# Kernel tuning notes

Hardware: AMD Instinct MI355X
Metric: run time of the kernel (lower is better)

Reference implementation:

```python
import jax, jax.numpy as jnp
import numpy as np

B, N = 64, 512
D_ENT, H = 2000, 768
LN_EPS = 1e-12


def setup_inputs() -> dict:
    key = jax.random.key(0)
    ks = jax.random.split(key, 16)
    s = 1.0 / np.sqrt(D_ENT)
    sh = 1.0 / np.sqrt(H)
    return {
        "node_embeddings": jax.random.normal(ks[0], (B, N, D_ENT), jnp.float32),
        "node_types": jax.random.randint(ks[1], (B, N), 0, 2),
        "layers": jax.random.randint(ks[2], (B, N), 0, 8),
        "operators": jax.random.randint(ks[3], (B, N), 0, 2),
        "in_degs": jax.random.randint(ks[4], (B, N), 0, 8),
        "out_degs": jax.random.randint(ks[5], (B, N), 0, 8),
        "negs": jax.random.randint(ks[6], (B, N), 0, 2),
        "type_emb": jax.random.normal(ks[7], (2, H), jnp.float32),
        "layer_emb": jax.random.normal(ks[8], (8, H), jnp.float32),
        "op_emb": jax.random.normal(ks[9], (2, H), jnp.float32),
        "in_emb": jax.random.normal(ks[10], (8, H), jnp.float32),
        "out_emb": jax.random.normal(ks[11], (8, H), jnp.float32),
        "proj_w": jax.random.uniform(ks[12], (H, D_ENT), jnp.float32, -s, s),
        "proj_b": jnp.zeros((H,), jnp.float32),
        "neg_w": jax.random.uniform(ks[13], (H, H), jnp.float32, -sh, sh),
        "neg_b": jnp.zeros((H,), jnp.float32),
        "ln_g": jnp.ones((H,), jnp.float32),
        "ln_b": jnp.zeros((H,), jnp.float32),
    }


def reference(node_embeddings, node_types, layers, operators, in_degs, out_degs, negs,
              type_emb, layer_emb, op_emb, in_emb, out_emb,
              proj_w, proj_b, neg_w, neg_b, ln_g, ln_b):
    # linear projection: [B,N,D_ENT] @ [D_ENT,H]
    x = jnp.einsum("bnd,hd->bnh", node_embeddings, proj_w) + proj_b
    # summed small-table lookups
    x = x + type_emb[node_types] + layer_emb[layers] + op_emb[operators] \
        + in_emb[in_degs] + out_emb[out_degs]
    # rows with negs==1 go through MLP (single Linear h->h); masked select/scatter
    y = jnp.einsum("bnh,gh->bng", x, neg_w) + neg_b
    x = jnp.where((negs == 1)[..., None], y, x)
    # LayerNorm
    mu = jnp.mean(x, axis=-1, keepdims=True)
    var = jnp.mean(jnp.square(x - mu), axis=-1, keepdims=True)
    x = (x - mu) * jax.lax.rsqrt(var + LN_EPS) * ln_g + ln_b
    # dropout is identity in eval mode
    return x
```

## Files before the change

kernel.cpp:

```cpp
#include <hip/hip_runtime.h>
#include <stdint.h>

typedef unsigned short u16;
typedef short v8s __attribute__((ext_vector_type(8)));
typedef float v4f __attribute__((ext_vector_type(4)));

typedef __attribute__((address_space(1))) uint32_t g_u32;
typedef __attribute__((address_space(3))) uint32_t l_u32;

__device__ __forceinline__ void glds16(const void* g, void* l) {
    __builtin_amdgcn_global_load_lds((const g_u32*)g, (l_u32*)l, 16, 0, 0);
}

__device__ __forceinline__ u16 f2b(float f) {
    uint32_t u = __builtin_bit_cast(uint32_t, f);
    u += 0x7FFFu + ((u >> 16) & 1u);
    return (u16)(u >> 16);
}

__device__ __forceinline__ uint32_t pk2(float a, float b) {
    uint32_t ua = __builtin_bit_cast(uint32_t, a) + 0x8000u;
    uint32_t ub = __builtin_bit_cast(uint32_t, b) + 0x8000u;
    return __builtin_amdgcn_perm(ub, ua, 0x07060302u);
}

#define MTOT  32768
#define HDIM  768
#define KDIM  2000
#define KPAD  2016

__global__ __launch_bounds__(256) void cvt_weights(
    const float* __restrict__ pw, const float* __restrict__ nw,
    u16* __restrict__ Wb, u16* __restrict__ NWb)
{
    const int h = blockIdx.x;
    const float* src = pw + (size_t)h * KDIM;
    u16* dst = Wb + (size_t)h * KPAD;
    for (int k = threadIdx.x; k < KPAD; k += 256)
        dst[k] = (k < KDIM) ? f2b(src[k]) : (u16)0;
    const float* s2 = nw + (size_t)h * HDIM;
    u16* d2 = NWb + (size_t)h * HDIM;
    for (int k = threadIdx.x; k < HDIM; k += 256)
        d2[k] = f2b(s2[k]);
}

__global__ __launch_bounds__(512, 2) void gemm1(
    const float* __restrict__ A, const u16* __restrict__ Wb,
    const float* __restrict__ pb,
    const int* __restrict__ i_ty, const int* __restrict__ i_la,
    const int* __restrict__ i_op, const int* __restrict__ i_in, const int* __restrict__ i_ou,
    const float* __restrict__ te, const float* __restrict__ le, const float* __restrict__ oe,
    const float* __restrict__ ie, const float* __restrict__ ooe,
    u16* __restrict__ Xb)
{
    __shared__ __align__(16) float Asf[3][256 * 32];
    __shared__ __align__(16) u16  Bs[3][256 * 32];

    const int bid = blockIdx.x;
    const int s = bid >> 3;
    const int mt = (bid & 7) * 16 + s / 3;
    const int nt = s % 3;
    const int m_base = mt * 256, n_base = nt * 256;

    const int tid = threadIdx.x;
    const int w = tid >> 6, lane = tid & 63;
    const int lm = lane & 15, quad = lane >> 4;
    const int wm = (w >> 2) * 128, wn = (w & 3) * 64;

    const float* aRowBase[4];
    int aOff[4];
    int aBase[4];
#pragma unroll
    for (int t = 0; t < 4; t++) {
        const int rl = w * 32 + t * 8 + (lane >> 3);
        const int c16 = (lane & 7) ^ (rl & 7);
        aRowBase[t] = A + (size_t)(m_base + rl) * KDIM;
        aOff[t] = c16 * 4;
        aBase[t] = (w * 32 + t * 8) * 32;
    }
    const u16* bSrc[2];
    int bBase[2];
#pragma unroll
    for (int t = 0; t < 2; t++) {
        const int rl = w * 32 + t * 16 + (lane >> 2);
        const int c = (lane & 3) ^ ((rl >> 1) & 3);
        bSrc[t] = Wb + (size_t)(n_base + rl) * KPAD + c * 8;
        bBase[t] = (w * 32 + t * 16) * 32;
    }

    v4f acc[8][4];
#pragma unroll
    for (int i = 0; i < 8; i++)
#pragma unroll
        for (int j = 0; j < 4; j++) acc[i][j] = (v4f){0.f, 0.f, 0.f, 0.f};

    auto issue = [&](int kb) {
        const int sl = kb % 3;
#pragma unroll
        for (int t = 0; t < 4; t++) {
            int k = kb * 32 + aOff[t];
            k = (k > 1996) ? 1996 : k;
            glds16(aRowBase[t] + k, &Asf[sl][aBase[t]]);
        }
#pragma unroll
        for (int t = 0; t < 2; t++)
            glds16(bSrc[t] + kb * 32, &Bs[sl][bBase[t]]);
    };

    auto compute = [&](int kb) {
        const int sl = kb % 3;
        v8s af[8], bf[4];
#pragma unroll
        for (int i = 0; i < 8; i++) {
            const int r = wm + i * 16 + lm;
            const int sw = r & 7;
            const float4 lo = *(const float4*)&Asf[sl][r * 32 + (((2 * quad)     ^ sw) << 2)];
            const float4 hi = *(const float4*)&Asf[sl][r * 32 + (((2 * quad + 1) ^ sw) << 2)];
            int4 p;
            p.x = (int)pk2(lo.x, lo.y); p.y = (int)pk2(lo.z, lo.w);
            p.z = (int)pk2(hi.x, hi.y); p.w = (int)pk2(hi.z, hi.w);
            af[i] = __builtin_bit_cast(v8s, p);
        }
#pragma unroll
        for (int j = 0; j < 4; j++) {
            const int r = wn + j * 16 + lm;
            bf[j] = *(const v8s*)&Bs[sl][r * 32 + ((quad ^ ((r >> 1) & 3)) << 3)];
        }
#pragma unroll
        for (int i = 0; i < 8; i++)
#pragma unroll
            for (int j = 0; j < 4; j++)
                acc[i][j] = __builtin_amdgcn_mfma_f32_16x16x32_bf16(af[i], bf[j], acc[i][j], 0, 0, 0);
    };

    issue(0);
    issue(1);

    for (int kb = 0; kb < 61; ++kb) {
        asm volatile("s_waitcnt vmcnt(6)" ::: "memory");
        __builtin_amdgcn_s_barrier();
        __builtin_amdgcn_sched_barrier(0);
        issue(kb + 2);
        compute(kb);
    }
    asm volatile("s_waitcnt vmcnt(6)" ::: "memory");
    __builtin_amdgcn_s_barrier();
    __builtin_amdgcn_sched_barrier(0);
    compute(61);
    asm volatile("s_waitcnt vmcnt(0)" ::: "memory");
    __builtin_amdgcn_s_barrier();
    __builtin_amdgcn_sched_barrier(0);
    compute(62);

#pragma unroll
    for (int i = 0; i < 8; i++) {
#pragma unroll
        for (int r = 0; r < 4; r++) {
            const int row = m_base + wm + i * 16 + quad * 4 + r;
            const int ty = i_ty[row], la = i_la[row], op = i_op[row];
            const int di = i_in[row], doo = i_ou[row];
            const float* pte = te + (size_t)ty * HDIM;
            const float* ple = le + (size_t)la * HDIM;
            const float* poe = oe + (size_t)op * HDIM;
            const float* pie = ie + (size_t)di * HDIM;
            const float* pou = ooe + (size_t)doo * HDIM;
            u16* orow = Xb + (size_t)row * HDIM;
#pragma unroll
            for (int j = 0; j < 4; j++) {
                const int col = n_base + wn + j * 16 + lm;
                float v = acc[i][j][r] + pb[col] + pte[col] + ple[col] + poe[col] + pie[col] + pou[col];
                orow[col] = f2b(v);
            }
        }
    }
}

__global__ __launch_bounds__(512, 2) void gemm2(
    const u16* __restrict__ Xb, const u16* __restrict__ NWb,
    const float* __restrict__ nb, u16* __restrict__ Yb)
{
    __shared__ __align__(16) u16 As[3][256 * 32];
    __shared__ __align__(16) u16 Bs[3][256 * 32];

    const int bid = blockIdx.x;
    const int s = bid >> 3;
    const int mt = (bid & 7) * 16 + s / 3;
    const int nt = s % 3;
    const int m_base = mt * 256, n_base = nt * 256;

    const int tid = threadIdx.x;
    const int w = tid >> 6, lane = tid & 63;
    const int lm = lane & 15, quad = lane >> 4;
    const int wm = (w >> 2) * 128, wn = (w & 3) * 64;

    const u16* aSrc[2];
    const u16* bSrc[2];
    int sBase[2];
#pragma unroll
    for (int t = 0; t < 2; t++) {
        const int rl = w * 32 + t * 16 + (lane >> 2);
        const int c = (lane & 3) ^ ((rl >> 1) & 3);
        aSrc[t] = Xb  + (size_t)(m_base + rl) * HDIM + c * 8;
        bSrc[t] = NWb + (size_t)(n_base + rl) * HDIM + c * 8;
        sBase[t] = (w * 32 + t * 16) * 32;
    }

    v4f acc[8][4];
#pragma unroll
    for (int i = 0; i < 8; i++)
#pragma unroll
        for (int j = 0; j < 4; j++) acc[i][j] = (v4f){0.f, 0.f, 0.f, 0.f};

    auto issue = [&](int kb) {
        const int sl = kb % 3;
#pragma unroll
        for (int t = 0; t < 2; t++) {
            glds16(aSrc[t] + kb * 32, &As[sl][sBase[t]]);
            glds16(bSrc[t] + kb * 32, &Bs[sl][sBase[t]]);
        }
    };

    auto compute = [&](int kb) {
        const int sl = kb % 3;
        v8s af[8], bf[4];
#pragma unroll
        for (int i = 0; i < 8; i++) {
            const int r = wm + i * 16 + lm;
            af[i] = *(const v8s*)&As[sl][r * 32 + ((quad ^ ((r >> 1) & 3)) << 3)];
        }
#pragma unroll
        for (int j = 0; j < 4; j++) {
            const int r = wn + j * 16 + lm;
            bf[j] = *(const v8s*)&Bs[sl][r * 32 + ((quad ^ ((r >> 1) & 3)) << 3)];
        }
#pragma unroll
        for (int i = 0; i < 8; i++)
#pragma unroll
            for (int j = 0; j < 4; j++)
                acc[i][j] = __builtin_amdgcn_mfma_f32_16x16x32_bf16(af[i], bf[j], acc[i][j], 0, 0, 0);
    };

    issue(0);
    issue(1);

    for (int kb = 0; kb < 22; ++kb) {
        asm volatile("s_waitcnt vmcnt(4)" ::: "memory");
        __builtin_amdgcn_s_barrier();
        __builtin_amdgcn_sched_barrier(0);
        issue(kb + 2);
        compute(kb);
    }
    asm volatile("s_waitcnt vmcnt(4)" ::: "memory");
    __builtin_amdgcn_s_barrier();
    __builtin_amdgcn_sched_barrier(0);
    compute(22);
    asm volatile("s_waitcnt vmcnt(0)" ::: "memory");
    __builtin_amdgcn_s_barrier();
    __builtin_amdgcn_sched_barrier(0);
    compute(23);

#pragma unroll
    for (int i = 0; i < 8; i++) {
#pragma unroll
        for (int r = 0; r < 4; r++) {
            const int row = m_base + wm + i * 16 + quad * 4 + r;
            u16* orow = Yb + (size_t)row * HDIM;
#pragma unroll
            for (int j = 0; j < 4; j++) {
                const int col = n_base + wn + j * 16 + lm;
                orow[col] = f2b(acc[i][j][r] + nb[col]);
            }
        }
    }
}

__global__ __launch_bounds__(256) void ln_k(
    const u16* __restrict__ Xb, const u16* __restrict__ Yb,
    const int* __restrict__ negs,
    const float* __restrict__ g, const float* __restrict__ b,
    float* __restrict__ out)
{
    const int w = threadIdx.x >> 6, lane = threadIdx.x & 63;
    const int row = blockIdx.x * 4 + w;
    const u16* src = ((negs[row] == 1) ? Yb : Xb) + (size_t)row * HDIM;

    float v[12];
    float s = 0.f, ss = 0.f;
#pragma unroll
    for (int p = 0; p < 3; p++) {
        uint2 u = *(const uint2*)(src + (p * 64 + lane) * 4);
        float f0 = __builtin_bit_cast(float, u.x << 16);
        float f1 = __builtin_bit_cast(float, u.x & 0xFFFF0000u);
        float f2 = __builtin_bit_cast(float, u.y << 16);
        float f3 = __builtin_bit_cast(float, u.y & 0xFFFF0000u);
        v[p * 4 + 0] = f0; v[p * 4 + 1] = f1; v[p * 4 + 2] = f2; v[p * 4 + 3] = f3;
        s += f0 + f1 + f2 + f3;
        ss += f0 * f0 + f1 * f1 + f2 * f2 + f3 * f3;
    }
#pragma unroll
    for (int off = 1; off < 64; off <<= 1) {
        s += __shfl_xor(s, off);
        ss += __shfl_xor(ss, off);
    }
    const float mean = s * (1.f / (float)HDIM);
    const float var = ss * (1.f / (float)HDIM) - mean * mean;
    const float rs = rsqrtf(var + 1e-12f);

    float* orow = out + (size_t)row * HDIM;
#pragma unroll
    for (int p = 0; p < 3; p++) {
        const int c0 = (p * 64 + lane) * 4;
        float4 gg = *(const float4*)(g + c0);
        float4 bb = *(const float4*)(b + c0);
        float4 o;
        o.x = (v[p * 4 + 0] - mean) * rs * gg.x + bb.x;
        o.y = (v[p * 4 + 1] - mean) * rs * gg.y + bb.y;
        o.z = (v[p * 4 + 2] - mean) * rs * gg.z + bb.z;
        o.w = (v[p * 4 + 3] - mean) * rs * gg.w + bb.w;
        *(float4*)(orow + c0) = o;
    }
}

extern "C" void kernel_launch(void* const* d_in, const int* in_sizes, int n_in,
                              void* d_out, int out_size, void* d_ws, size_t ws_size,
                              hipStream_t stream) {
    (void)in_sizes; (void)n_in; (void)out_size; (void)ws_size;
    const float* A   = (const float*)d_in[0];
    const int* i_ty  = (const int*)d_in[1];
    const int* i_la  = (const int*)d_in[2];
    const int* i_op  = (const int*)d_in[3];
    const int* i_in  = (const int*)d_in[4];
    const int* i_ou  = (const int*)d_in[5];
    const int* negs  = (const int*)d_in[6];
    const float* te  = (const float*)d_in[7];
    const float* le  = (const float*)d_in[8];
    const float* oe  = (const float*)d_in[9];
    const float* ie  = (const float*)d_in[10];
    const float* ooe = (const float*)d_in[11];
    const float* pw  = (const float*)d_in[12];
    const float* pb  = (const float*)d_in[13];
    const float* nw  = (const float*)d_in[14];
    const float* nb  = (const float*)d_in[15];
    const float* lng = (const float*)d_in[16];
    const float* lnb = (const float*)d_in[17];
    float* out = (float*)d_out;

    char* ws = (char*)d_ws;
    u16* Wb  = (u16*)ws;
    u16* NWb = (u16*)(ws + 3096576);
    u16* Xb  = (u16*)(ws + 3096576 + 1179648);
    u16* Yb  = (u16*)(ws + 3096576 + 1179648 + 50331648);

    cvt_weights<<<768, 256, 0, stream>>>(pw, nw, Wb, NWb);
    gemm1<<<384, 512, 0, stream>>>(A, Wb, pb, i_ty, i_la, i_op, i_in, i_ou,
                                   te, le, oe, ie, ooe, Xb);
    gemm2<<<384, 512, 0, stream>>>(Xb, NWb, nb, Yb);
    ln_k<<<8192, 256, 0, stream>>>(Xb, Yb, negs, lng, lnb, out);
}
```

Baseline: 773.2 us.

## Restructure both GEMMs into 8-phase double-buffered K=64 pipelines with register-staged A conversion

Both GEMM kernels move from a triple-buffered K=32 loop to double-buffered K=64 tiles, and each K-step is split into quadrant phases that interleave loads with MFMA bursts raised with s_setprio. In gemm1 the fp32 A tile is now loaded into registers and converted to bf16 once before the LDS write, instead of staging fp32 in LDS and packing at every fragment read. This halves A's LDS footprint and conversion traffic. Weight padding grows to 2048 so K tiles align, and block-to-tile swizzling changes. The cost is more registers for staged A, more barriers per tile, and a hand-tuned vmcnt schedule that could be fragile.

```diff
diff --git a/kernel.cpp b/kernel.cpp
--- a/kernel.cpp
+++ b/kernel.cpp
@@ -11,13 +11,11 @@
 __device__ __forceinline__ void glds16(const void* g, void* l) {
     __builtin_amdgcn_global_load_lds((const g_u32*)g, (l_u32*)l, 16, 0, 0);
 }
-
 __device__ __forceinline__ u16 f2b(float f) {
     uint32_t u = __builtin_bit_cast(uint32_t, f);
     u += 0x7FFFu + ((u >> 16) & 1u);
     return (u16)(u >> 16);
 }
-
 __device__ __forceinline__ uint32_t pk2(float a, float b) {
     uint32_t ua = __builtin_bit_cast(uint32_t, a) + 0x8000u;
     uint32_t ub = __builtin_bit_cast(uint32_t, b) + 0x8000u;
@@ -27,7 +25,11 @@
 #define MTOT  32768
 #define HDIM  768
 #define KDIM  2000
-#define KPAD  2016
+#define KP2   2048
+
+#define BARX do { __builtin_amdgcn_s_barrier(); __builtin_amdgcn_sched_barrier(0); } while (0)
+#define VMW(n) asm volatile("s_waitcnt vmcnt(" #n ")" ::: "memory")
+#define LGKM0  asm volatile("s_waitcnt lgkmcnt(0)" ::: "memory")
 
 __global__ __launch_bounds__(256) void cvt_weights(
     const float* __restrict__ pw, const float* __restrict__ nw,
@@ -35,8 +37,8 @@
 {
     const int h = blockIdx.x;
     const float* src = pw + (size_t)h * KDIM;
-    u16* dst = Wb + (size_t)h * KPAD;
-    for (int k = threadIdx.x; k < KPAD; k += 256)
+    u16* dst = Wb + (size_t)h * KP2;
+    for (int k = threadIdx.x; k < KP2; k += 256)
         dst[k] = (k < KDIM) ? f2b(src[k]) : (u16)0;
     const float* s2 = nw + (size_t)h * HDIM;
     u16* d2 = NWb + (size_t)h * HDIM;
@@ -53,13 +55,12 @@
     const float* __restrict__ ie, const float* __restrict__ ooe,
     u16* __restrict__ Xb)
 {
-    __shared__ __align__(16) float Asf[3][256 * 32];
-    __shared__ __align__(16) u16  Bs[3][256 * 32];
+    __shared__ __align__(16) u16 As[2][256 * 64];
+    __shared__ __align__(16) u16 Bs[2][256 * 64];
 
     const int bid = blockIdx.x;
-    const int s = bid >> 3;
-    const int mt = (bid & 7) * 16 + s / 3;
-    const int nt = s % 3;
+    const int sw = (bid & 7) * 48 + (bid >> 3);
+    const int mt = sw / 3, nt = sw % 3;
     const int m_base = mt * 256, n_base = nt * 256;
 
     const int tid = threadIdx.x;
@@ -67,26 +68,10 @@
     const int lm = lane & 15, quad = lane >> 4;
     const int wm = (w >> 2) * 128, wn = (w & 3) * 64;
 
-    const float* aRowBase[4];
-    int aOff[4];
-    int aBase[4];
-#pragma unroll
-    for (int t = 0; t < 4; t++) {
-        const int rl = w * 32 + t * 8 + (lane >> 3);
-        const int c16 = (lane & 7) ^ (rl & 7);
-        aRowBase[t] = A + (size_t)(m_base + rl) * KDIM;
-        aOff[t] = c16 * 4;
-        aBase[t] = (w * 32 + t * 8) * 32;
-    }
-    const u16* bSrc[2];
-    int bBase[2];
-#pragma unroll
-    for (int t = 0; t < 2; t++) {
-        const int rl = w * 32 + t * 16 + (lane >> 2);
-        const int c = (lane & 3) ^ ((rl >> 1) & 3);
-        bSrc[t] = Wb + (size_t)(n_base + rl) * KPAD + c * 8;
-        bBase[t] = (w * 32 + t * 16) * 32;
-    }
+    const int rsub = lane >> 3, csub = lane & 7;
+    const int cxa = csub ^ (rsub & 7);
+    const float* aBase = A + (size_t)(m_base + rsub) * KDIM;
+    const u16* bBase = Wb + (size_t)(n_base + rsub) * KP2 + cxa * 8;
 
     v4f acc[8][4];
 #pragma unroll
@@ -94,63 +79,88 @@
 #pragma unroll
         for (int j = 0; j < 4; j++) acc[i][j] = (v4f){0.f, 0.f, 0.f, 0.f};
 
-    auto issue = [&](int kb) {
-        const int sl = kb % 3;
-#pragma unroll
-        for (int t = 0; t < 4; t++) {
-            int k = kb * 32 + aOff[t];
-            k = (k > 1996) ? 1996 : k;
-            glds16(aRowBase[t] + k, &Asf[sl][aBase[t]]);
-        }
-#pragma unroll
-        for (int t = 0; t < 2; t++)
-            glds16(bSrc[t] + kb * 32, &Bs[sl][bBase[t]]);
-    };
-
-    auto compute = [&](int kb) {
-        const int sl = kb % 3;
-        v8s af[8], bf[4];
-#pragma unroll
-        for (int i = 0; i < 8; i++) {
-            const int r = wm + i * 16 + lm;
-            const int sw = r & 7;
-            const float4 lo = *(const float4*)&Asf[sl][r * 32 + (((2 * quad)     ^ sw) << 2)];
-            const float4 hi = *(const float4*)&Asf[sl][r * 32 + (((2 * quad + 1) ^ sw) << 2)];
-            int4 p;
-            p.x = (int)pk2(lo.x, lo.y); p.y = (int)pk2(lo.z, lo.w);
-            p.z = (int)pk2(hi.x, hi.y); p.w = (int)pk2(hi.z, hi.w);
-            af[i] = __builtin_bit_cast(v8s, p);
-        }
-#pragma unroll
-        for (int j = 0; j < 4; j++) {
-            const int r = wn + j * 16 + lm;
-            bf[j] = *(const v8s*)&Bs[sl][r * 32 + ((quad ^ ((r >> 1) & 3)) << 3)];
-        }
-#pragma unroll
-        for (int i = 0; i < 8; i++)
-#pragma unroll
-            for (int j = 0; j < 4; j++)
-                acc[i][j] = __builtin_amdgcn_mfma_f32_16x16x32_bf16(af[i], bf[j], acc[i][j], 0, 0, 0);
-    };
-
-    issue(0);
-    issue(1);
-
-    for (int kb = 0; kb < 61; ++kb) {
-        asm volatile("s_waitcnt vmcnt(6)" ::: "memory");
-        __builtin_amdgcn_s_barrier();
+    auto ldA = [&](int kt, int g, float4* r) {
+        int ko = kt * 64 + cxa * 8;
+        if (ko > 1992) ko = 1992;
+#pragma unroll
+        for (int h = 0; h < 2; h++) {
+            const float* p = aBase + (size_t)(g * 64 + w * 8 + h * 128) * KDIM + ko;
+            r[h * 2 + 0] = *(const float4*)p;
+            r[h * 2 + 1] = *(const float4*)(p + 4);
+        }
+    };
+    auto wrA = [&](int buf, int g, const float4* r) {
+#pragma unroll
+        for (int h = 0; h < 2; h++) {
+            const int row = g * 64 + w * 8 + h * 128 + rsub;
+            int4 q;
+            q.x = (int)pk2(r[h*2].x, r[h*2].y);   q.y = (int)pk2(r[h*2].z, r[h*2].w);
+            q.z = (int)pk2(r[h*2+1].x, r[h*2+1].y); q.w = (int)pk2(r[h*2+1].z, r[h*2+1].w);
+            *(int4*)&As[buf][row * 64 + csub * 8] = q;
+        }
+    };
+    auto stB = [&](int kt, int s, int buf) {
+#pragma unroll
+        for (int h = 0; h < 2; h++) {
+            const int rowb = s * 32 + (w >> 2) * 64 + (w & 3) * 8 + h * 128;
+            glds16(bBase + (size_t)rowb * KP2 + kt * 64, &Bs[buf][rowb * 64]);
+        }
+    };
+    auto phase = [&](int buf, int qm, int qn) {
+        v8s af[4][2], bf[2][2];
+#pragma unroll
+        for (int fi = 0; fi < 4; fi++)
+#pragma unroll
+            for (int ks = 0; ks < 2; ks++) {
+                const int r = wm + qm * 64 + fi * 16 + lm;
+                af[fi][ks] = *(const v8s*)&As[buf][r * 64 + (((ks * 4 + quad) ^ (lm & 7)) << 3)];
+            }
+#pragma unroll
+        for (int fj = 0; fj < 2; fj++)
+#pragma unroll
+            for (int ks = 0; ks < 2; ks++) {
+                const int r = wn + qn * 32 + fj * 16 + lm;
+                bf[fj][ks] = *(const v8s*)&Bs[buf][r * 64 + (((ks * 4 + quad) ^ (lm & 7)) << 3)];
+            }
+        LGKM0;
         __builtin_amdgcn_sched_barrier(0);
-        issue(kb + 2);
-        compute(kb);
-    }
-    asm volatile("s_waitcnt vmcnt(6)" ::: "memory");
-    __builtin_amdgcn_s_barrier();
-    __builtin_amdgcn_sched_barrier(0);
-    compute(61);
-    asm volatile("s_waitcnt vmcnt(0)" ::: "memory");
-    __builtin_amdgcn_s_barrier();
-    __builtin_amdgcn_sched_barrier(0);
-    compute(62);
+        __builtin_amdgcn_s_setprio(1);
+#pragma unroll
+        for (int fi = 0; fi < 4; fi++)
+#pragma unroll
+            for (int fj = 0; fj < 2; fj++)
+#pragma unroll
+                for (int ks = 0; ks < 2; ks++)
+                    acc[qm*4+fi][qn*2+fj] = __builtin_amdgcn_mfma_f32_16x16x32_bf16(
+                        af[fi][ks], bf[fj][ks], acc[qm*4+fi][qn*2+fj], 0, 0, 0);
+        __builtin_amdgcn_s_setprio(0);
+    };
+
+    float4 r0[4], r1[4], r2[4], sPrev[4];
+    ldA(0, 0, r0); ldA(0, 1, r1); ldA(1, 0, r2);
+    stB(0, 0, 0);
+    VMW(10); wrA(0, 0, r0);
+    VMW(6);  wrA(0, 1, r1);
+    VMW(2);  wrA(1, 0, r2);
+    stB(0, 1, 0);
+    ldA(1, 1, sPrev);
+    stB(1, 0, 1);
+    LGKM0;
+
+    for (int it = 0; it < 16; ++it) {
+        int tO1 = 2 * it + 1;
+        int tE2 = 2 * it + 2; if (tE2 > 31) tE2 = 31;
+        int tO3 = 2 * it + 3; if (tO3 > 31) tO3 = 31;
+        float4 s0[4], s1[4], s2[4];
+        BARX; ldA(tE2, 0, s0); VMW(6); wrA(1, 1, sPrev); phase(0, 0, 0);
+        BARX; stB(tO1, 1, 1); phase(0, 0, 1);
+        BARX; ldA(tE2, 1, s1); VMW(6); wrA(0, 0, s0); phase(0, 1, 0);
+        BARX; stB(tE2, 0, 0); phase(0, 1, 1);
+        BARX; ldA(tO3, 0, s2); VMW(6); wrA(0, 1, s1); phase(1, 0, 0);
+        BARX; stB(tE2, 1, 0); phase(1, 0, 1);
+        BARX; ldA(tO3, 1, sPrev); VMW(6); wrA(1, 0, s2); phase(1, 1, 0);
+        BARX; stB(tO3, 0, 1); phase(1, 1, 1);
+    }
 
 #pragma unroll
     for (int i = 0; i < 8; i++) {
@@ -179,13 +189,12 @@
     const u16* __restrict__ Xb, const u16* __restrict__ NWb,
     const float* __restrict__ nb, u16* __restrict__ Yb)
 {
-    __shared__ __align__(16) u16 As[3][256 * 32];
-    __shared__ __align__(16) u16 Bs[3][256 * 32];
+    __shared__ __align__(16) u16 As[2][256 * 64];
+    __shared__ __align__(16) u16 Bs[2][256 * 64];
 
     const int bid = blockIdx.x;
-    const int s = bid >> 3;
-    const int mt = (bid & 7) * 16 + s / 3;
-    const int nt = s % 3;
+    const int sw = (bid & 7) * 48 + (bid >> 3);
+    const int mt = sw / 3, nt = sw % 3;
     const int m_base = mt * 256, n_base = nt * 256;
 
     const int tid = threadIdx.x;
@@ -193,17 +202,10 @@
     const int lm = lane & 15, quad = lane >> 4;
     const int wm = (w >> 2) * 128, wn = (w & 3) * 64;
 
-    const u16* aSrc[2];
-    const u16* bSrc[2];
-    int sBase[2];
-#pragma unroll
-    for (int t = 0; t < 2; t++) {
-        const int rl = w * 32 + t * 16 + (lane >> 2);
-        const int c = (lane & 3) ^ ((rl >> 1) & 3);
-        aSrc[t] = Xb  + (size_t)(m_base + rl) * HDIM + c * 8;
-        bSrc[t] = NWb + (size_t)(n_base + rl) * HDIM + c * 8;
-        sBase[t] = (w * 32 + t * 16) * 32;
-    }
+    const int rsub = lane >> 3, csub = lane & 7;
+    const int cxa = csub ^ (rsub & 7);
+    const u16* aBase = Xb  + (size_t)(m_base + rsub) * HDIM + cxa * 8;
+    const u16* bBase = NWb + (size_t)(n_base + rsub) * HDIM + cxa * 8;
 
     v4f acc[8][4];
 #pragma unroll
@@ -211,53 +213,66 @@
 #pragma unroll
         for (int j = 0; j < 4; j++) acc[i][j] = (v4f){0.f, 0.f, 0.f, 0.f};
 
-    auto issue = [&](int kb) {
-        const int sl = kb % 3;
-#pragma unroll
-        for (int t = 0; t < 2; t++) {
-            glds16(aSrc[t] + kb * 32, &As[sl][sBase[t]]);
-            glds16(bSrc[t] + kb * 32, &Bs[sl][sBase[t]]);
-        }
-    };
-
-    auto compute = [&](int kb) {
-        const int sl = kb % 3;
-        v8s af[8], bf[4];
-#pragma unroll
-        for (int i = 0; i < 8; i++) {
-            const int r = wm + i * 16 + lm;
-            af[i] = *(const v8s*)&As[sl][r * 32 + ((quad ^ ((r >> 1) & 3)) << 3)];
-        }
-#pragma unroll
-        for (int j = 0; j < 4; j++) {
-            const int r = wn + j * 16 + lm;
-            bf[j] = *(const v8s*)&Bs[sl][r * 32 + ((quad ^ ((r >> 1) & 3)) << 3)];
-        }
-#pragma unroll
-        for (int i = 0; i < 8; i++)
-#pragma unroll
-            for (int j = 0; j < 4; j++)
-                acc[i][j] = __builtin_amdgcn_mfma_f32_16x16x32_bf16(af[i], bf[j], acc[i][j], 0, 0, 0);
-    };
-
-    issue(0);
-    issue(1);
-
-    for (int kb = 0; kb < 22; ++kb) {
-        asm volatile("s_waitcnt vmcnt(4)" ::: "memory");
-        __builtin_amdgcn_s_barrier();
+    auto stA = [&](int kt, int g, int buf) {
+#pragma unroll
+        for (int h = 0; h < 2; h++) {
+            const int rowb = g * 64 + w * 8 + h * 128;
+            glds16(aBase + (size_t)rowb * HDIM + kt * 64, &As[buf][rowb * 64]);
+        }
+    };
+    auto stB = [&](int kt, int s, int buf) {
+#pragma unroll
+        for (int h = 0; h < 2; h++) {
+            const int rowb = s * 32 + (w >> 2) * 64 + (w & 3) * 8 + h * 128;
+            glds16(bBase + (size_t)rowb * HDIM + kt * 64, &Bs[buf][rowb * 64]);
+        }
+    };
+    auto phase = [&](int buf, int qm, int qn) {
+        v8s af[4][2], bf[2][2];
+#pragma unroll
+        for (int fi = 0; fi < 4; fi++)
+#pragma unroll
+            for (int ks = 0; ks < 2; ks++) {
+                const int r = wm + qm * 64 + fi * 16 + lm;
+                af[fi][ks] = *(const v8s*)&As[buf][r * 64 + (((ks * 4 + quad) ^ (lm & 7)) << 3)];
+            }
+#pragma unroll
+        for (int fj = 0; fj < 2; fj++)
+#pragma unroll
+            for (int ks = 0; ks < 2; ks++) {
+                const int r = wn + qn * 32 + fj * 16 + lm;
+                bf[fj][ks] = *(const v8s*)&Bs[buf][r * 64 + (((ks * 4 + quad) ^ (lm & 7)) << 3)];
+            }
+        LGKM0;
         __builtin_amdgcn_sched_barrier(0);
-        issue(kb + 2);
-        compute(kb);
-    }
-    asm volatile("s_waitcnt vmcnt(4)" ::: "memory");
-    __builtin_amdgcn_s_barrier();
-    __builtin_amdgcn_sched_barrier(0);
-    compute(22);
-    asm volatile("s_waitcnt vmcnt(0)" ::: "memory");
-    __builtin_amdgcn_s_barrier();
-    __builtin_amdgcn_sched_barrier(0);
-    compute(23);
+        __builtin_amdgcn_s_setprio(1);
+#pragma unroll
+        for (int fi = 0; fi < 4; fi++)
+#pragma unroll
+            for (int fj = 0; fj < 2; fj++)
+#pragma unroll
+                for (int ks = 0; ks < 2; ks++)
+                    acc[qm*4+fi][qn*2+fj] = __builtin_amdgcn_mfma_f32_16x16x32_bf16(
+                        af[fi][ks], bf[fj][ks], acc[qm*4+fi][qn*2+fj], 0, 0, 0);
+        __builtin_amdgcn_s_setprio(0);
+    };
+
+    stA(0, 0, 0); stB(0, 0, 0); stA(0, 1, 0); stB(0, 1, 0);
+    stA(1, 0, 1); stB(1, 0, 1);
+
+    for (int it = 0; it < 6; ++it) {
+        int tO1 = 2 * it + 1;
+        int tE2 = 2 * it + 2; if (tE2 > 11) tE2 = 11;
+        int tO3 = 2 * it + 3; if (tO3 > 11) tO3 = 11;
+        BARX; VMW(8); stA(tO1, 1, 1); phase(0, 0, 0);
+        BARX; VMW(6); stB(tO1, 1, 1); phase(0, 0, 1);
+        BARX; stA(tE2, 0, 0); phase(0, 1, 0);
+        BARX; stB(tE2, 0, 0); phase(0, 1, 1);
+        BARX; VMW(8); stA(tE2, 1, 0); phase(1, 0, 0);
+        BARX; VMW(6); stB(tE2, 1, 0); phase(1, 0, 1);
+        BARX; stA(tO3, 0, 1); phase(1, 1, 0);
+        BARX; stB(tO3, 0, 1); phase(1, 1, 1);
+    }
 
 #pragma unroll
     for (int i = 0; i < 8; i++) {
@@ -347,9 +362,9 @@
 
     char* ws = (char*)d_ws;
     u16* Wb  = (u16*)ws;
-    u16* NWb = (u16*)(ws + 3096576);
-    u16* Xb  = (u16*)(ws + 3096576 + 1179648);
-    u16* Yb  = (u16*)(ws + 3096576 + 1179648 + 50331648);
+    u16* NWb = (u16*)(ws + 3145728);
+    u16* Xb  = (u16*)(ws + 3145728 + 1179648);
+    u16* Yb  = (u16*)(ws + 3145728 + 1179648 + 50331648);
 
     cvt_weights<<<768, 256, 0, stream>>>(pw, nw, Wb, NWb);
     gemm1<<<384, 512, 0, stream>>>(A, Wb, pb, i_ty, i_la, i_op, i_in, i_ou,
```

Result: faster. 685.6 us (-11.3%).
